# Optimization experiments

Measured on AMD Instinct MI355X. Metric: run time of the kernel, lower is better.

Reference implementation:

```python
import jax, jax.numpy as jnp
import numpy as np

D_MODEL = 1024
N_HEADS = 16
FFN_DIM = 4096
EPS = 1e-5


def layer_norm(x, g, b):
    m = jnp.mean(x, axis=-1, keepdims=True)
    v = jnp.mean((x - m) ** 2, axis=-1, keepdims=True)
    return (x - m) * jax.lax.rsqrt(v + EPS) * g + b


def setup_inputs() -> dict:
    key = jax.random.key(0)
    ks = jax.random.split(key, 8)
    B, S, D, F = 4, 1024, D_MODEL, FFN_DIM
    return {
        "k": jax.random.normal(ks[0], (B, S, D), jnp.float32),
        "v": jax.random.normal(ks[1], (B, S, D), jnp.float32),
        "q": jax.random.normal(ks[2], (B, S, D), jnp.float32),
        "r": jax.random.normal(ks[3], (B, S, D), jnp.float32),
        "Wf": jax.random.normal(ks[4], (D, D), jnp.float32) * 0.02,
        "bf": jnp.zeros((D,), jnp.float32),
        "g1": jnp.ones((D,), jnp.float32),
        "b1": jnp.zeros((D,), jnp.float32),
        "W1": jax.random.normal(ks[5], (D, F), jnp.float32) * 0.02,
        "bw1": jnp.zeros((F,), jnp.float32),
        "W2": jax.random.normal(ks[6], (F, D), jnp.float32) * 0.02,
        "bw2": jnp.zeros((D,), jnp.float32),
        "g2": jnp.ones((D,), jnp.float32),
        "b2": jnp.zeros((D,), jnp.float32),
    }


def reference(k, v, q, r, Wf, bf, g1, b1, W1, bw1, W2, bw2, g2, b2):
    B, S, D = k.shape
    H = N_HEADS
    d = D // H
    # Encoder layer calls attention(k, q, v, r) against signature (k, v, q, r):
    # inner_q = outer v, inner_v = outer q  (faithful to the source quirk).
    kk = k.reshape(B * H, -1, d)   # raw view-based head split, as in torch
    vv = q.reshape(B * H, -1, d)
    qq = v.reshape(B * H, -1, d)
    scale = d ** 0.5  # NOTE: source MULTIPLIES by sqrt(d)
    scores = jnp.einsum('bqd,bkd->bqk', qq, kk) * scale  # [B*H, S, S]
    attn = jax.nn.softmax(scores, axis=-1)
    ctx = jnp.einsum('bqk,bkd->bqd', attn, vv).reshape(B, -1, D)
    out = ctx @ Wf + bf
    x = layer_norm(r + out, g1, b1)
    # FFN: 1x1 Conv1d pair == dense matmuls
    h = jax.nn.relu(x @ W1 + bw1)
    y = h @ W2 + bw2
    output = layer_norm(x + y, g2, b2)
    return (output, attn)
```

## Files before the change

### kernel.cpp

```cpp
#include <hip/hip_runtime.h>
#include <hip/hip_bf16.h>
#include <cstdint>

typedef __attribute__((ext_vector_type(8))) __bf16 bf16x8;
typedef __attribute__((ext_vector_type(4))) __bf16 bf16x4;
typedef __attribute__((ext_vector_type(4))) float f32x4;
typedef unsigned int uint32;
typedef unsigned short uint16;

#define LDS_AS __attribute__((address_space(3)))
#define GLB_AS __attribute__((address_space(1)))

static __device__ __forceinline__ void gld_lds16(const void* g, LDS_AS char* l) {
  __builtin_amdgcn_global_load_lds((const GLB_AS uint32*)g, (LDS_AS uint32*)l, 16, 0, 0);
}

#define MFMA(a, b, c) __builtin_amdgcn_mfma_f32_16x16x32_bf16((a), (b), (c), 0, 0, 0)

static __device__ __forceinline__ f32x4 mfma3(bf16x8 ah, bf16x8 al, bf16x8 bh,
                                              bf16x8 bl, f32x4 c) {
  c = MFMA(ah, bh, c);
  c = MFMA(al, bh, c);
  c = MFMA(ah, bl, c);
  return c;
}

static __device__ __forceinline__ uint32 pack_bf16(float a, float b) {
  __bf16 ha = (__bf16)a, hb = (__bf16)b;
  return (uint32)__builtin_bit_cast(uint16, ha) |
         ((uint32)__builtin_bit_cast(uint16, hb) << 16);
}

#define KB(row, colbyte) ((((row) * 128 + (colbyte))) ^ (((row) & 7) << 4))

__global__ __launch_bounds__(256) void prep_all(
    const float* __restrict__ K, const float* __restrict__ V,
    char* __restrict__ KH, char* __restrict__ KL, char* __restrict__ VT,
    const float* __restrict__ Wf, __bf16* __restrict__ WFT,
    const float* __restrict__ W1, __bf16* __restrict__ W1T,
    const float* __restrict__ W2, __bf16* __restrict__ W2T) {
  int b = blockIdx.x;
  if (b < 1024) {
    int kt = b & 15, h = b >> 4;
    const float* src = K + (size_t)h * 65536 + kt * 4096;
    char* dh = KH + (size_t)(h * 16 + kt) * 8192;
    char* dl = KL + (size_t)(h * 16 + kt) * 8192;
    int r = threadIdx.x >> 2, cq = threadIdx.x & 3;
    const float* sp = src + r * 64 + cq * 16;
    bf16x8 h0, l0, h1, l1;
#pragma unroll
    for (int j = 0; j < 8; ++j) {
      float x0 = sp[j], x1 = sp[8 + j];
      __bf16 a = (__bf16)x0, bb = (__bf16)x1;
      h0[j] = a; l0[j] = (__bf16)(x0 - (float)a);
      h1[j] = bb; l1[j] = (__bf16)(x1 - (float)bb);
    }
    int sw = (r & 7) << 4;
    int o0 = (r * 128 + cq * 32) ^ sw;
    int o1 = (r * 128 + cq * 32 + 16) ^ sw;
    *(bf16x8*)(dh + o0) = h0;
    *(bf16x8*)(dh + o1) = h1;
    *(bf16x8*)(dl + o0) = l0;
    *(bf16x8*)(dl + o1) = l1;
    return;
  }
  if (b < 2048) {
    b -= 1024;
    int kt = b & 15, h = b >> 4;
    const float* src = V + (size_t)h * 65536 + kt * 4096;
    char* dv = VT + (size_t)(h * 16 + kt) * 8192;
    int kp = threadIdx.x >> 3, dq = threadIdx.x & 7;
    const float* s0 = src + (2 * kp) * 64 + dq * 8;
    const float* s1 = s0 + 64;
#pragma unroll
    for (int j = 0; j < 8; ++j) {
      uint32 pk = pack_bf16(s0[j], s1[j]);
      int d = dq * 8 + j;
      *(uint32*)(dv + ((d * 128 + kp * 4) ^ ((d & 7) << 4))) = pk;
    }
    return;
  }
  const float* in;
  __bf16* out;
  int R, C, bx, by;
  if (b < 3072) {
    b -= 2048; in = Wf; out = WFT; R = 1024; C = 1024;
    bx = (b & 31) * 32; by = (b >> 5) * 32;
  } else if (b < 7168) {
    b -= 3072; in = W1; out = W1T; R = 1024; C = 4096;
    bx = (b & 127) * 32; by = (b >> 7) * 32;
  } else {
    b -= 7168; in = W2; out = W2T; R = 4096; C = 1024;
    bx = (b & 31) * 32; by = (b >> 5) * 32;
  }
  __shared__ float tile[32][33];
  int tx = threadIdx.x & 31, ty = threadIdx.x >> 5;
  for (int i = ty; i < 32; i += 8)
    tile[i][tx] = in[(size_t)(by + i) * C + bx + tx];
  __syncthreads();
  for (int i = ty; i < 32; i += 8)
    out[(size_t)(bx + i) * R + by + tx] = (__bf16)tile[tx][i];
}

__global__ __launch_bounds__(512, 4) void attn_v8(
    const float* __restrict__ Qin, const char* __restrict__ KHimg,
    const char* __restrict__ KLimg, const char* __restrict__ VTimg,
    float* __restrict__ attn_out, __bf16* __restrict__ ctx_out)
{
  __shared__ __attribute__((aligned(16))) char KsH[2][8192];
  __shared__ __attribute__((aligned(16))) char KsL[2][8192];
  __shared__ __attribute__((aligned(16))) char Vt[2][8192];
  __shared__ __attribute__((aligned(16))) __bf16 PsH[8][16][72];

  const int tid = threadIdx.x;
  const int l = tid & 63, w = tid >> 6;
  const int lr = l & 15, q4 = l >> 4;
  const int swz = (blockIdx.x & 7) * 64 + (blockIdx.x >> 3);
  const int g = swz >> 3, rb = swz & 7;
  const size_t base = (size_t)g * 65536;
  const char* khb = KHimg + (size_t)g * 131072;
  const char* klb = KLimg + (size_t)g * 131072;
  const char* vtb = VTimg + (size_t)g * 131072;

  const float* qp = Qin + base + (size_t)(rb * 128 + w * 16 + lr) * 64;
  f32x4 qv[4];
#pragma unroll
  for (int j = 0; j < 2; ++j) {
    qv[j] = *(const f32x4*)&qp[q4 * 8 + j * 4];
    qv[2 + j] = *(const f32x4*)&qp[32 + q4 * 8 + j * 4];
  }

  gld_lds16(khb + 0 * 8192 + tid * 16, (LDS_AS char*)&KsH[0][0] + tid * 16);
  gld_lds16(klb + 0 * 8192 + tid * 16, (LDS_AS char*)&KsL[0][0] + tid * 16);

  bf16x8 aqh0, aql0, aqh1, aql1;
#pragma unroll
  for (int j = 0; j < 8; ++j) {
    float x0 = qv[j >> 2][j & 3];
    float x1 = qv[2 + (j >> 2)][j & 3];
    __bf16 h0 = (__bf16)x0, h1 = (__bf16)x1;
    aqh0[j] = h0; aql0[j] = (__bf16)(x0 - (float)h0);
    aqh1[j] = h1; aql1[j] = (__bf16)(x1 - (float)h1);
  }

  float m_r[4], ll_r[4];
#pragma unroll
  for (int r = 0; r < 4; ++r) { m_r[r] = -1e30f; ll_r[r] = 0.f; }

  for (int kt = 0; kt < 16; ++kt) {
    const int buf = kt & 1;
    if (kt < 15) {
      gld_lds16(khb + (kt + 1) * 8192 + tid * 16,
                (LDS_AS char*)&KsH[buf ^ 1][0] + tid * 16);
      gld_lds16(klb + (kt + 1) * 8192 + tid * 16,
                (LDS_AS char*)&KsL[buf ^ 1][0] + tid * 16);
      asm volatile("s_waitcnt vmcnt(2)" ::: "memory");
    } else {
      asm volatile("s_waitcnt vmcnt(0)" ::: "memory");
    }
    __builtin_amdgcn_s_barrier();
    const char* ksh = KsH[buf];
    const char* ksl = KsL[buf];
    f32x4 c[4];
#pragma unroll
    for (int nf = 0; nf < 4; ++nf) {
      int row = nf * 16 + lr;
      f32x4 cc = {0.f, 0.f, 0.f, 0.f};
      cc = mfma3(aqh0, aql0, *(const bf16x8*)(ksh + KB(row, q4 * 16)),
                 *(const bf16x8*)(ksl + KB(row, q4 * 16)), cc);
      cc = mfma3(aqh1, aql1, *(const bf16x8*)(ksh + KB(row, 64 + q4 * 16)),
                 *(const bf16x8*)(ksl + KB(row, 64 + q4 * 16)), cc);
      c[nf] = cc;
    }
#pragma unroll
    for (int r = 0; r < 4; ++r) {
      float s0 = c[0][r] * 8.f, s1 = c[1][r] * 8.f;
      float s2 = c[2][r] * 8.f, s3 = c[3][r] * 8.f;
      float lm = fmaxf(fmaxf(s0, s1), fmaxf(s2, s3));
      float mnew = fmaxf(m_r[r], lm);
      ll_r[r] = ll_r[r] * __expf(m_r[r] - mnew) +
                (__expf(s0 - mnew) + __expf(s1 - mnew) +
                 __expf(s2 - mnew) + __expf(s3 - mnew));
      m_r[r] = mnew;
    }
    __builtin_amdgcn_s_barrier();
  }
  float inv_l[4];
#pragma unroll
  for (int r = 0; r < 4; ++r) {
    float M = m_r[r];
#pragma unroll
    for (int o = 1; o < 16; o <<= 1) M = fmaxf(M, __shfl_xor(M, o, 64));
    float ls = ll_r[r] * __expf(m_r[r] - M);
#pragma unroll
    for (int o = 1; o < 16; o <<= 1) ls += __shfl_xor(ls, o, 64);
    m_r[r] = M;
    inv_l[r] = 1.f / ls;
  }

  f32x4 co[4];
#pragma unroll
  for (int cf = 0; cf < 4; ++cf) co[cf] = (f32x4){0.f, 0.f, 0.f, 0.f};

  gld_lds16(khb + 0 * 8192 + tid * 16, (LDS_AS char*)&KsH[0][0] + tid * 16);
  gld_lds16(klb + 0 * 8192 + tid * 16, (LDS_AS char*)&KsL[0][0] + tid * 16);
  gld_lds16(vtb + 0 * 8192 + tid * 16, (LDS_AS char*)&Vt[0][0] + tid * 16);

  for (int kt = 0; kt < 16; ++kt) {
    const int buf = kt & 1;
    if (kt < 15) {
      gld_lds16(khb + (kt + 1) * 8192 + tid * 16,
                (LDS_AS char*)&KsH[buf ^ 1][0] + tid * 16);
      gld_lds16(klb + (kt + 1) * 8192 + tid * 16,
                (LDS_AS char*)&KsL[buf ^ 1][0] + tid * 16);
      gld_lds16(vtb + (kt + 1) * 8192 + tid * 16,
                (LDS_AS char*)&Vt[buf ^ 1][0] + tid * 16);
    }
    if (kt == 0) {
      asm volatile("s_waitcnt vmcnt(3)" ::: "memory");
    } else if (kt < 15) {
      asm volatile("s_waitcnt vmcnt(19)" ::: "memory");
    } else {
      asm volatile("s_waitcnt vmcnt(16)" ::: "memory");
    }
    __builtin_amdgcn_s_barrier();
    const char* ksh = KsH[buf];
    const char* ksl = KsL[buf];
    const char* vts = Vt[buf];
#pragma unroll
    for (int nf = 0; nf < 4; ++nf) {
      int row = nf * 16 + lr;
      f32x4 cc = {0.f, 0.f, 0.f, 0.f};
      cc = mfma3(aqh0, aql0, *(const bf16x8*)(ksh + KB(row, q4 * 16)),
                 *(const bf16x8*)(ksl + KB(row, q4 * 16)), cc);
      cc = mfma3(aqh1, aql1, *(const bf16x8*)(ksh + KB(row, 64 + q4 * 16)),
                 *(const bf16x8*)(ksl + KB(row, 64 + q4 * 16)), cc);
#pragma unroll
      for (int r = 0; r < 4; ++r) {
        float p = __expf(cc[r] * 8.f - m_r[r]) * inv_l[r];
        PsH[w][q4 * 4 + r][nf * 16 + lr] = (__bf16)p;
        int arow = rb * 128 + w * 16 + q4 * 4 + r;
        __builtin_nontemporal_store(
            p, &attn_out[((size_t)(g * 1024 + arow)) * 1024 + kt * 64 + nf * 16 + lr]);
      }
    }
#pragma unroll
    for (int kk = 0; kk < 2; ++kk) {
      bf16x8 ph = *(const bf16x8*)&PsH[w][lr][kk * 32 + q4 * 8];
#pragma unroll
      for (int cf = 0; cf < 4; ++cf) {
        bf16x8 vt = *(const bf16x8*)(vts + KB(cf * 16 + lr, kk * 64 + q4 * 16));
        co[cf] = MFMA(ph, vt, co[cf]);
      }
    }
    __builtin_amdgcn_s_barrier();
  }
#pragma unroll
  for (int cf = 0; cf < 4; ++cf)
#pragma unroll
    for (int r = 0; r < 4; ++r) {
      int i = rb * 128 + w * 16 + q4 * 4 + r;
      ctx_out[((size_t)(g * 1024 + i)) * 64 + cf * 16 + lr] = (__bf16)co[cf][r];
    }
}

template <int EPI, int BM>
__global__ __launch_bounds__(256) void gemm_db(
    const __bf16* __restrict__ A, const __bf16* __restrict__ Bt,
    const float* __restrict__ bias, const float* __restrict__ Res,
    float* __restrict__ Outf, __bf16* __restrict__ Outb,
    int M, int N, int K, int Kloop, int nbx, int tiles_per_out)
{
  constexpr int MF = BM / 32;
  constexpr int ELEMS = BM * 64 + 8192;
  __shared__ __attribute__((aligned(16))) __bf16 sm[2][ELEMS];
  const int tid = threadIdx.x;
  const int l = tid & 63, w = tid >> 6;
  const int lr = l & 15, lkb = (l >> 4) * 8;
  const int nwg = gridDim.x;
  const int swz = (blockIdx.x & 7) * (nwg >> 3) + (blockIdx.x >> 3);
  const int ks = swz / tiles_per_out;
  const int tile = swz % tiles_per_out;
  const int m0 = (tile / nbx) * BM, n0 = (tile % nbx) * 128;
  const int kbase = ks * Kloop;
  const int wr = (w >> 1) * (BM / 2), wc = (w & 1) * 64;

  f32x4 acc[MF][4];
  f32x4 zero = {0.f, 0.f, 0.f, 0.f};
#pragma unroll
  for (int m = 0; m < MF; ++m)
#pragma unroll
    for (int n = 0; n < 4; ++n) acc[m][n] = zero;

  const int nkt = Kloop >> 6;

#define GSTAGE(BUF, KT)                                                        \
  {                                                                            \
    LDS_AS char* dst = (LDS_AS char*)&sm[(BUF)][0];                            \
    _Pragma("unroll") for (int it = 0; it < MF; ++it) {                        \
      int slot = it * 256 + tid;                                               \
      int row = slot >> 3, cb = slot & 7;                                      \
      gld_lds16(&A[(size_t)(m0 + row) * K + kbase + (KT) * 64 + cb * 8],       \
                dst + slot * 16);                                              \
    }                                                                          \
    _Pragma("unroll") for (int it = 0; it < 4; ++it) {                         \
      int slot = it * 256 + tid;                                               \
      int row = slot >> 3, cb = slot & 7;                                      \
      gld_lds16(&Bt[(size_t)(n0 + row) * K + kbase + (KT) * 64 + cb * 8],      \
                dst + BM * 128 + slot * 16);                                   \
    }                                                                          \
  }

  GSTAGE(0, 0);
  for (int kt = 0; kt < nkt; ++kt) {
    const int buf = kt & 1;
    if (kt < nkt - 1) {
      GSTAGE(buf ^ 1, kt + 1);
      if (BM == 64) {
        asm volatile("s_waitcnt vmcnt(6)" ::: "memory");
      } else {
        asm volatile("s_waitcnt vmcnt(8)" ::: "memory");
      }
    } else {
      asm volatile("s_waitcnt vmcnt(0)" ::: "memory");
    }
    __builtin_amdgcn_s_barrier();
    const __bf16* s = &sm[buf][0];
#pragma unroll
    for (int kk = 0; kk < 2; ++kk) {
      bf16x8 a[MF], b[4];
#pragma unroll
      for (int m = 0; m < MF; ++m)
        a[m] = *(const bf16x8*)&s[(wr + m * 16 + lr) * 64 + kk * 32 + lkb];
#pragma unroll
      for (int n = 0; n < 4; ++n)
        b[n] = *(const bf16x8*)&s[BM * 64 + (wc + n * 16 + lr) * 64 + kk * 32 + lkb];
#pragma unroll
      for (int m = 0; m < MF; ++m)
#pragma unroll
        for (int n = 0; n < 4; ++n) acc[m][n] = MFMA(a[m], b[n], acc[m][n]);
    }
    __builtin_amdgcn_s_barrier();
  }
#undef GSTAGE

  float* outp = (EPI == 3) ? Outf + (size_t)ks * M * N : Outf;
#pragma unroll
  for (int n = 0; n < 4; ++n) {
    int gcol = n0 + wc + n * 16 + lr;
    float bc = (EPI == 3) ? 0.f : bias[gcol];
#pragma unroll
    for (int m = 0; m < MF; ++m) {
      int grow = m0 + wr + m * 16 + (l >> 4) * 4;
#pragma unroll
      for (int r = 0; r < 4; ++r) {
        float v = acc[m][n][r] + bc;
        size_t o = (size_t)(grow + r) * N + gcol;
        if (EPI == 4) {
          Outb[o] = (__bf16)(v + Res[o]);
        } else {
          outp[o] = v;
        }
      }
    }
  }
}

template <int EPI, int BM>
__global__ __launch_bounds__(256) void gemm_bt(
    const __bf16* __restrict__ A, const __bf16* __restrict__ Bt,
    const float* __restrict__ bias, __bf16* __restrict__ Outb,
    int M, int N, int K, int nbx)
{
  constexpr int MF = BM / 32;
  __shared__ __attribute__((aligned(16))) __bf16 sm[BM * 64 + 8192];
  const int tid = threadIdx.x;
  const int l = tid & 63, w = tid >> 6;
  const int lr = l & 15, lkb = (l >> 4) * 8;
  const int nwg = gridDim.x;
  const int swz = (blockIdx.x & 7) * (nwg >> 3) + (blockIdx.x >> 3);
  const int m0 = (swz / nbx) * BM, n0 = (swz % nbx) * 128;
  const int wr = (w >> 1) * (BM / 2), wc = (w & 1) * 64;
  LDS_AS char* sm3 = (LDS_AS char*)sm;

  f32x4 acc[MF][4];
  f32x4 zero = {0.f, 0.f, 0.f, 0.f};
#pragma unroll
  for (int m = 0; m < MF; ++m)
#pragma unroll
    for (int n = 0; n < 4; ++n) acc[m][n] = zero;

  const int nkt = K >> 6;
  for (int kt = 0; kt < nkt; ++kt) {
    __syncthreads();
#pragma unroll
    for (int it = 0; it < MF; ++it) {
      int slot = it * 256 + tid;
      int row = slot >> 3, cb = slot & 7;
      gld_lds16(&A[(size_t)(m0 + row) * K + kt * 64 + cb * 8], sm3 + slot * 16);
    }
#pragma unroll
    for (int it = 0; it < 4; ++it) {
      int slot = it * 256 + tid;
      int row = slot >> 3, cb = slot & 7;
      gld_lds16(&Bt[(size_t)(n0 + row) * K + kt * 64 + cb * 8],
                sm3 + BM * 128 + slot * 16);
    }
    __syncthreads();
#pragma unroll
    for (int kk = 0; kk < 2; ++kk) {
      bf16x8 a[MF], b[4];
#pragma unroll
      for (int m = 0; m < MF; ++m)
        a[m] = *(const bf16x8*)&sm[(wr + m * 16 + lr) * 64 + kk * 32 + lkb];
#pragma unroll
      for (int n = 0; n < 4; ++n)
        b[n] = *(const bf16x8*)&sm[BM * 64 + (wc + n * 16 + lr) * 64 + kk * 32 + lkb];
#pragma unroll
      for (int m = 0; m < MF; ++m)
#pragma unroll
        for (int n = 0; n < 4; ++n) acc[m][n] = MFMA(a[m], b[n], acc[m][n]);
    }
  }

#pragma unroll
  for (int n = 0; n < 4; ++n) {
    int gcol = n0 + wc + n * 16 + lr;
    float bc = bias[gcol];
#pragma unroll
    for (int m = 0; m < MF; ++m) {
      int grow = m0 + wr + m * 16 + (l >> 4) * 4;
#pragma unroll
      for (int r = 0; r < 4; ++r) {
        float v = acc[m][n][r] + bc;
        size_t o = (size_t)(grow + r) * N + gcol;
        Outb[o] = (__bf16)fmaxf(v, 0.f);
      }
    }
  }
}

__global__ __launch_bounds__(256) void ln_b2b(
    const __bf16* __restrict__ in, const float* __restrict__ gam,
    const float* __restrict__ bet, __bf16* __restrict__ outB)
{
  __shared__ float red[8];
  const int row = blockIdx.x, t = threadIdx.x;
  bf16x4 vb = ((const bf16x4*)(in + (size_t)row * 1024))[t];
  float v[4];
  float s = 0.f, ss = 0.f;
#pragma unroll
  for (int j = 0; j < 4; ++j) {
    v[j] = (float)vb[j];
    s += v[j];
    ss += v[j] * v[j];
  }
#pragma unroll
  for (int o = 1; o < 64; o <<= 1) {
    s += __shfl_xor(s, o, 64);
    ss += __shfl_xor(ss, o, 64);
  }
  int w = t >> 6, l = t & 63;
  if (l == 0) { red[w] = s; red[4 + w] = ss; }
  __syncthreads();
  float S = red[0] + red[1] + red[2] + red[3];
  float SS = red[4] + red[5] + red[6] + red[7];
  float mean = S * (1.f / 1024.f);
  float var = SS * (1.f / 1024.f) - mean * mean;
  float rstd = rsqrtf(var + 1e-5f);
  bf16x4 ob;
#pragma unroll
  for (int j = 0; j < 4; ++j) {
    int col = t * 4 + j;
    ob[j] = (__bf16)((v[j] - mean) * rstd * gam[col] + bet[col]);
  }
  ((bf16x4*)(outB + (size_t)row * 1024))[t] = ob;
}

__global__ __launch_bounds__(256) void ln_fuse2(
    const float* __restrict__ P0, const float* __restrict__ P1,
    const float* __restrict__ bias, const __bf16* __restrict__ resB,
    const float* __restrict__ gam, const float* __restrict__ bet,
    float* __restrict__ out)
{
  __shared__ float red[8];
  const int row = blockIdx.x, t = threadIdx.x;
  const size_t ro = (size_t)row * 1024;
  f32x4 v = ((const f32x4*)(P0 + ro))[t];
  f32x4 v1 = ((const f32x4*)(P1 + ro))[t];
  f32x4 bi = ((const f32x4*)bias)[t];
  bf16x4 rb = ((const bf16x4*)(resB + ro))[t];
  float s = 0.f, ss = 0.f;
#pragma unroll
  for (int j = 0; j < 4; ++j) {
    v[j] = v[j] + v1[j] + bi[j] + (float)rb[j];
    s += v[j];
    ss += v[j] * v[j];
  }
#pragma unroll
  for (int o = 1; o < 64; o <<= 1) {
    s += __shfl_xor(s, o, 64);
    ss += __shfl_xor(ss, o, 64);
  }
  int w = t >> 6, l = t & 63;
  if (l == 0) { red[w] = s; red[4 + w] = ss; }
  __syncthreads();
  float S = red[0] + red[1] + red[2] + red[3];
  float SS = red[4] + red[5] + red[6] + red[7];
  float mean = S * (1.f / 1024.f);
  float var = SS * (1.f / 1024.f) - mean * mean;
  float rstd = rsqrtf(var + 1e-5f);
  f32x4 ov;
#pragma unroll
  for (int j = 0; j < 4; ++j) {
    int col = t * 4 + j;
    ov[j] = (v[j] - mean) * rstd * gam[col] + bet[col];
  }
  ((f32x4*)(out + ro))[t] = ov;
}

extern "C" void kernel_launch(void* const* d_in, const int* in_sizes, int n_in,
                              void* d_out, int out_size, void* d_ws, size_t ws_size,
                              hipStream_t stream) {
  const float* k_in = (const float*)d_in[0];
  const float* v_in = (const float*)d_in[1];
  const float* q_in = (const float*)d_in[2];
  const float* r_in = (const float*)d_in[3];
  const float* Wf = (const float*)d_in[4];
  const float* bf = (const float*)d_in[5];
  const float* g1 = (const float*)d_in[6];
  const float* b1 = (const float*)d_in[7];
  const float* W1 = (const float*)d_in[8];
  const float* bw1 = (const float*)d_in[9];
  const float* W2 = (const float*)d_in[10];
  const float* bw2 = (const float*)d_in[11];
  const float* g2 = (const float*)d_in[12];
  const float* b2 = (const float*)d_in[13];

  float* out0 = (float*)d_out;
  float* attn = out0 + 4194304;

  char* W = (char*)d_ws;
  const size_t MB = 1024 * 1024;
  char* KHimg = W + 0;
  char* KLimg = W + 8 * MB;
  char* VTimg = W + 16 * MB;
  __bf16* WFT = (__bf16*)(W + 24 * MB);
  __bf16* W1T = (__bf16*)(W + 26 * MB);
  __bf16* W2T = (__bf16*)(W + 34 * MB);
  __bf16* CTX = (__bf16*)(W + 42 * MB);
  __bf16* Xb = (__bf16*)(W + 50 * MB);
  __bf16* Hb = (__bf16*)(W + 58 * MB);
  __bf16* T1b = (__bf16*)(W + 90 * MB);
  float* P0 = (float*)(W + 106 * MB);
  float* P1 = (float*)(W + 122 * MB);

  prep_all<<<11264, 256, 0, stream>>>(k_in, q_in, KHimg, KLimg, VTimg,
                                      Wf, WFT, W1, W1T, W2, W2T);

  attn_v8<<<512, 512, 0, stream>>>(v_in, KHimg, KLimg, VTimg, attn, CTX);

  gemm_db<4, 64><<<512, 256, 0, stream>>>(CTX, WFT, bf, r_in, nullptr, T1b,
                                          4096, 1024, 1024, 1024, 8, 512);
  ln_b2b<<<4096, 256, 0, stream>>>(T1b, g1, b1, Xb);
  gemm_bt<1, 128><<<1024, 256, 0, stream>>>(Xb, W1T, bw1, Hb, 4096, 4096, 1024, 32);
  gemm_db<3, 128><<<512, 256, 0, stream>>>(Hb, W2T, nullptr, nullptr, P0, nullptr,
                                           4096, 1024, 4096, 2048, 8, 256);
  ln_fuse2<<<4096, 256, 0, stream>>>(P0, P1, bw2, Xb, g2, b2, out0);
}
```

Before: 280.8 us.

## Use double-buffered GEMM for FFN1 and store split-K partials in bf16

Replaces the single-buffered gemm_bt used for the first FFN matmul with the double-buffered gemm_db kernel, adding a ReLU epilogue mode. The second FFN matmul's split-K partial outputs are now written as bf16 instead of fp32, and the final layer-norm kernel reads them as bf16. This aims to overlap global loads with MFMA work in FFN1 and halve partial-sum memory traffic, at the cost of rounding the partial sums to bf16 before reduction.

```diff
diff --git a/kernel.cpp b/kernel.cpp
--- a/kernel.cpp
+++ b/kernel.cpp
@@ -268,7 +268,7 @@
 __global__ __launch_bounds__(256) void gemm_db(
     const __bf16* __restrict__ A, const __bf16* __restrict__ Bt,
     const float* __restrict__ bias, const float* __restrict__ Res,
-    float* __restrict__ Outf, __bf16* __restrict__ Outb,
+    __bf16* __restrict__ Outb,
     int M, int N, int K, int Kloop, int nbx, int tiles_per_out)
 {
   constexpr int MF = BM / 32;
@@ -344,11 +344,11 @@
   }
 #undef GSTAGE
 
-  float* outp = (EPI == 3) ? Outf + (size_t)ks * M * N : Outf;
+  __bf16* outp = (EPI == 5) ? Outb + (size_t)ks * M * N : Outb;
 #pragma unroll
   for (int n = 0; n < 4; ++n) {
     int gcol = n0 + wc + n * 16 + lr;
-    float bc = (EPI == 3) ? 0.f : bias[gcol];
+    float bc = (EPI == 5) ? 0.f : bias[gcol];
 #pragma unroll
     for (int m = 0; m < MF; ++m) {
       int grow = m0 + wr + m * 16 + (l >> 4) * 4;
@@ -356,85 +356,13 @@
       for (int r = 0; r < 4; ++r) {
         float v = acc[m][n][r] + bc;
         size_t o = (size_t)(grow + r) * N + gcol;
-        if (EPI == 4) {
-          Outb[o] = (__bf16)(v + Res[o]);
+        if (EPI == 1) {
+          outp[o] = (__bf16)fmaxf(v, 0.f);
+        } else if (EPI == 4) {
+          outp[o] = (__bf16)(v + Res[o]);
         } else {
-          outp[o] = v;
+          outp[o] = (__bf16)v;
         }
-      }
-    }
-  }
-}
-
-template <int EPI, int BM>
-__global__ __launch_bounds__(256) void gemm_bt(
-    const __bf16* __restrict__ A, const __bf16* __restrict__ Bt,
-    const float* __restrict__ bias, __bf16* __restrict__ Outb,
-    int M, int N, int K, int nbx)
-{
-  constexpr int MF = BM / 32;
-  __shared__ __attribute__((aligned(16))) __bf16 sm[BM * 64 + 8192];
-  const int tid = threadIdx.x;
-  const int l = tid & 63, w = tid >> 6;
-  const int lr = l & 15, lkb = (l >> 4) * 8;
-  const int nwg = gridDim.x;
-  const int swz = (blockIdx.x & 7) * (nwg >> 3) + (blockIdx.x >> 3);
-  const int m0 = (swz / nbx) * BM, n0 = (swz % nbx) * 128;
-  const int wr = (w >> 1) * (BM / 2), wc = (w & 1) * 64;
-  LDS_AS char* sm3 = (LDS_AS char*)sm;
-
-  f32x4 acc[MF][4];
-  f32x4 zero = {0.f, 0.f, 0.f, 0.f};
-#pragma unroll
-  for (int m = 0; m < MF; ++m)
-#pragma unroll
-    for (int n = 0; n < 4; ++n) acc[m][n] = zero;
-
-  const int nkt = K >> 6;
-  for (int kt = 0; kt < nkt; ++kt) {
-    __syncthreads();
-#pragma unroll
-    for (int it = 0; it < MF; ++it) {
-      int slot = it * 256 + tid;
-      int row = slot >> 3, cb = slot & 7;
-      gld_lds16(&A[(size_t)(m0 + row) * K + kt * 64 + cb * 8], sm3 + slot * 16);
-    }
-#pragma unroll
-    for (int it = 0; it < 4; ++it) {
-      int slot = it * 256 + tid;
-      int row = slot >> 3, cb = slot & 7;
-      gld_lds16(&Bt[(size_t)(n0 + row) * K + kt * 64 + cb * 8],
-                sm3 + BM * 128 + slot * 16);
-    }
-    __syncthreads();
-#pragma unroll
-    for (int kk = 0; kk < 2; ++kk) {
-      bf16x8 a[MF], b[4];
-#pragma unroll
-      for (int m = 0; m < MF; ++m)
-        a[m] = *(const bf16x8*)&sm[(wr + m * 16 + lr) * 64 + kk * 32 + lkb];
-#pragma unroll
-      for (int n = 0; n < 4; ++n)
-        b[n] = *(const bf16x8*)&sm[BM * 64 + (wc + n * 16 + lr) * 64 + kk * 32 + lkb];
-#pragma unroll
-      for (int m = 0; m < MF; ++m)
-#pragma unroll
-        for (int n = 0; n < 4; ++n) acc[m][n] = MFMA(a[m], b[n], acc[m][n]);
-    }
-  }
-
-#pragma unroll
-  for (int n = 0; n < 4; ++n) {
-    int gcol = n0 + wc + n * 16 + lr;
-    float bc = bias[gcol];
-#pragma unroll
-    for (int m = 0; m < MF; ++m) {
-      int grow = m0 + wr + m * 16 + (l >> 4) * 4;
-#pragma unroll
-      for (int r = 0; r < 4; ++r) {
-        float v = acc[m][n][r] + bc;
-        size_t o = (size_t)(grow + r) * N + gcol;
-        Outb[o] = (__bf16)fmaxf(v, 0.f);
       }
     }
   }
@@ -478,7 +406,7 @@
 }
 
 __global__ __launch_bounds__(256) void ln_fuse2(
-    const float* __restrict__ P0, const float* __restrict__ P1,
+    const __bf16* __restrict__ P0, const __bf16* __restrict__ P1,
     const float* __restrict__ bias, const __bf16* __restrict__ resB,
     const float* __restrict__ gam, const float* __restrict__ bet,
     float* __restrict__ out)
@@ -486,14 +414,15 @@
   __shared__ float red[8];
   const int row = blockIdx.x, t = threadIdx.x;
   const size_t ro = (size_t)row * 1024;
-  f32x4 v = ((const f32x4*)(P0 + ro))[t];
-  f32x4 v1 = ((const f32x4*)(P1 + ro))[t];
+  bf16x4 p0 = ((const bf16x4*)(P0 + ro))[t];
+  bf16x4 p1 = ((const bf16x4*)(P1 + ro))[t];
   f32x4 bi = ((const f32x4*)bias)[t];
   bf16x4 rb = ((const bf16x4*)(resB + ro))[t];
+  f32x4 v;
   float s = 0.f, ss = 0.f;
 #pragma unroll
   for (int j = 0; j < 4; ++j) {
-    v[j] = v[j] + v1[j] + bi[j] + (float)rb[j];
+    v[j] = (float)p0[j] + (float)p1[j] + bi[j] + (float)rb[j];
     s += v[j];
     ss += v[j] * v[j];
   }
@@ -552,19 +481,20 @@
   __bf16* Xb = (__bf16*)(W + 50 * MB);
   __bf16* Hb = (__bf16*)(W + 58 * MB);
   __bf16* T1b = (__bf16*)(W + 90 * MB);
-  float* P0 = (float*)(W + 106 * MB);
-  float* P1 = (float*)(W + 122 * MB);
+  __bf16* P0b = (__bf16*)(W + 98 * MB);
+  __bf16* P1b = (__bf16*)(W + 106 * MB);
 
   prep_all<<<11264, 256, 0, stream>>>(k_in, q_in, KHimg, KLimg, VTimg,
                                       Wf, WFT, W1, W1T, W2, W2T);
 
   attn_v8<<<512, 512, 0, stream>>>(v_in, KHimg, KLimg, VTimg, attn, CTX);
 
-  gemm_db<4, 64><<<512, 256, 0, stream>>>(CTX, WFT, bf, r_in, nullptr, T1b,
+  gemm_db<4, 64><<<512, 256, 0, stream>>>(CTX, WFT, bf, r_in, T1b,
                                           4096, 1024, 1024, 1024, 8, 512);
   ln_b2b<<<4096, 256, 0, stream>>>(T1b, g1, b1, Xb);
-  gemm_bt<1, 128><<<1024, 256, 0, stream>>>(Xb, W1T, bw1, Hb, 4096, 4096, 1024, 32);
-  gemm_db<3, 128><<<512, 256, 0, stream>>>(Hb, W2T, nullptr, nullptr, P0, nullptr,
+  gemm_db<1, 128><<<1024, 256, 0, stream>>>(Xb, W1T, bw1, nullptr, Hb,
+                                            4096, 4096, 1024, 1024, 32, 1024);
+  gemm_db<5, 128><<<512, 256, 0, stream>>>(Hb, W2T, nullptr, nullptr, P0b,
                                            4096, 1024, 4096, 2048, 8, 256);
-  ln_fuse2<<<4096, 256, 0, stream>>>(P0, P1, bw2, Xb, g2, b2, out0);
-}
+  ln_fuse2<<<4096, 256, 0, stream>>>(P0b, P1b, bw2, Xb, g2, b2, out0);
+}
```

Result: faster. 268.9 us (-4.3%).
